# Optimization experiments

Measured on AMD Instinct MI355X. Metric: run time of the kernel, lower is better.

Reference implementation:

```python
import jax, jax.numpy as jnp
import numpy as np

B = 32; SEQ = 900; GRID = 30; PFX = 16; D = 512
H = 8; HD = 64; WS = 3; SS = 1
NW = (GRID // WS) ** 2; N = WS * WS
INTER = 1536  # find_multiple(round(4.0*512*2/3), 256)
EPS = 1e-5
SCALE = HD ** -0.5


def _rel_pos_index():
    coords = np.stack(np.meshgrid(np.arange(WS), np.arange(WS), indexing='ij')).reshape(2, -1)
    rel = (coords[:, :, None] - coords[:, None, :]).transpose(1, 2, 0).copy()
    rel[:, :, 0] += WS - 1
    rel[:, :, 1] += WS - 1
    rel[:, :, 0] *= 2 * WS - 1
    return rel.sum(-1)  # [N, N]


def _attn_mask():
    img = np.zeros((GRID, GRID))
    cnt = 0
    sl = (slice(0, -WS), slice(-WS, -SS), slice(-SS, None))
    for h in sl:
        for w in sl:
            img[h, w] = cnt
            cnt += 1
    mw = img.reshape(GRID // WS, WS, GRID // WS, WS).transpose(0, 2, 1, 3).reshape(-1, N)
    diff = mw[:, None, :] - mw[:, :, None]
    return np.where(diff != 0, -100.0, 0.0).astype(np.float32)  # [nW, N, N]


REL_IDX = _rel_pos_index()
MASK = _attn_mask()


def rms_norm(x):
    xf = x.astype(jnp.float32)
    v = jnp.mean(xf * xf, -1, keepdims=True)
    return (xf * jax.lax.rsqrt(v + EPS)).astype(x.dtype)


def swiglu(x, gu_w, down_w):
    gu = x @ gu_w.T
    gate, up = gu[..., :INTER], gu[..., INTER:]
    return (jax.nn.silu(gate) * up) @ down_w.T


def setup_inputs() -> dict:
    key = jax.random.key(0)
    ks = jax.random.split(key, 8)
    s = 0.02
    return {
        'hidden_states': jax.random.normal(ks[0], (B, PFX + SEQ, D), jnp.float32),
        'qkv_w': jax.random.normal(ks[1], (3 * D, D), jnp.float32) * s,
        'qkv_b': jnp.zeros((3 * D,), jnp.float32),
        'proj_w': jax.random.normal(ks[2], (D, D), jnp.float32) * s,
        'proj_b': jnp.zeros((D,), jnp.float32),
        'rel_bias': jax.random.normal(ks[3], ((2 * WS - 1) ** 2, H), jnp.float32) * s,
        'gu_w': jax.random.normal(ks[4], (2 * INTER, D), jnp.float32) * s,
        'down_w': jax.random.normal(ks[5], (D, INTER), jnp.float32) * s,
        'pgu_w': jax.random.normal(ks[6], (2 * INTER, D), jnp.float32) * s,
        'pdown_w': jax.random.normal(ks[7], (D, INTER), jnp.float32) * s,
    }


def reference(hidden_states, qkv_w, qkv_b, proj_w, proj_b, rel_bias, gu_w, down_w, pgu_w, pdown_w):
    hs = hidden_states
    prefix = hs[:, :PFX]                                     # [B, 16, D]
    grid = hs[:, PFX:] + jnp.mean(prefix, 1, keepdims=True)  # broadcast prefix mean
    x = grid.reshape(B, GRID, GRID, D)
    residual = x
    # cyclic shift
    x = jnp.roll(x, (-SS, -SS), (1, 2))
    # window partition -> [B*nW, N, D]
    xw = x.reshape(B, GRID // WS, WS, GRID // WS, WS, D).transpose(0, 1, 3, 2, 4, 5).reshape(B * NW, N, D)
    qkv = (xw @ qkv_w.T + qkv_b).reshape(B * NW, N, 3, H, HD).transpose(2, 0, 3, 1, 4)
    q, k, v = qkv[0] * SCALE, qkv[1], qkv[2]                 # [B*nW, H, N, HD]
    attn = jnp.einsum('whid,whjd->whij', q, k)
    bias = rel_bias[jnp.asarray(REL_IDX).reshape(-1)].reshape(N, N, H).transpose(2, 0, 1)
    attn = attn + bias[None]
    attn = attn.reshape(B, NW, H, N, N) + jnp.asarray(MASK)[None, :, None]
    attn = jax.nn.softmax(attn.reshape(B * NW, H, N, N), -1)
    out = jnp.einsum('whij,whjd->whid', attn, v).transpose(0, 2, 1, 3).reshape(B * NW, N, D)
    out = out @ proj_w.T + proj_b
    # window reverse + reverse shift
    x = out.reshape(B, GRID // WS, GRID // WS, WS, WS, D).transpose(0, 1, 3, 2, 4, 5).reshape(B, GRID, GRID, D)
    x = jnp.roll(x, (SS, SS), (1, 2))
    x = rms_norm(residual.reshape(B, SEQ, D) + x.reshape(B, SEQ, D))
    prefix = rms_norm(prefix + swiglu(prefix, pgu_w, pdown_w))
    hs = jnp.concatenate([prefix, x], 1)
    return rms_norm(hs + swiglu(hs, gu_w, down_w))
```

## Files before the change

### kernel.cpp

```cpp
#include <hip/hip_runtime.h>
#include <cstdint>
#include <cstddef>

typedef float f32x4 __attribute__((ext_vector_type(4)));
typedef short s16x8 __attribute__((ext_vector_type(8)));
typedef short s16x4 __attribute__((ext_vector_type(4)));

#define DEV static __device__ __forceinline__

DEV float bf2f(short s) {
  union { unsigned u; float f; } c;
  c.u = ((unsigned)(unsigned short)s) << 16;
  return c.f;
}
DEV short f2bf(float f) {
  union { float f; unsigned u; } c;
  c.f = f;
  unsigned r = c.u + 0x7fffu + ((c.u >> 16) & 1u);
  return (short)(r >> 16);
}
DEV float wave_allsum(float v) {
#pragma unroll
  for (int off = 32; off > 0; off >>= 1) v += __shfl_xor(v, off, 64);
  return v;
}
DEV void gload_lds16(const void* g, void* l) {
  __builtin_amdgcn_global_load_lds(
      (const __attribute__((address_space(1))) void*)g,
      (__attribute__((address_space(3))) void*)l, 16, 0, 0);
}
DEV float silu_f(float g) { return g / (1.f + __expf(-g)); }

DEV int xcd_swizzle(int orig, int nwg) {
  int q = nwg >> 3, r = nwg & 7;
  int xcd = orig & 7, pos = orig >> 3;
  return (xcd < r ? xcd * (q + 1) : r * (q + 1) + (xcd - r) * q) + pos;
}

DEV void sync_phase() {
  asm volatile("s_waitcnt vmcnt(0)" ::: "memory");
  __builtin_amdgcn_s_barrier();
  __builtin_amdgcn_sched_barrier(0);
}

enum { EPI_BF16 = 0, EPI_BIAS_BF16 = 1, EPI_SCATTER = 4, EPI_ADDOUT = 5, EPI_GU = 6 };

template <int EPI>
__global__ __launch_bounds__(512, 2) void gemm8(
    const short* __restrict__ A, const short* __restrict__ W,
    const short* __restrict__ Wu, const float* __restrict__ bias,
    void* __restrict__ outp, int M, int N, int K)
{
  __shared__ short lds[65536];
  const int tid = threadIdx.x;
  const int wid = tid >> 6, lane = tid & 63;
  const int wr = wid >> 2, wc = wid & 3;
  const int nwg = gridDim.x * gridDim.y;
  const int orig = blockIdx.y * gridDim.x + blockIdx.x;
  const int wg = xcd_swizzle(orig, nwg);
  const int bx = wg % gridDim.x, by = wg / gridDim.x;
  const int row0 = by * 256;

  f32x4 acc[8][4];
#pragma unroll
  for (int m = 0; m < 8; ++m)
#pragma unroll
    for (int n = 0; n < 4; ++n) acc[m][n] = f32x4{0.f, 0.f, 0.f, 0.f};

  const int srow = tid >> 3;
  const int k8s = (tid & 7) ^ (srow & 7);
  const short* aub[4];
  const short* bub[4];
#pragma unroll
  for (int u = 0; u < 4; ++u)
    aub[u] = A + (size_t)(row0 + u * 64 + srow) * K + k8s * 8;
  if (EPI == EPI_GU) {
    const int colg = bx * 128;
#pragma unroll
    for (int u = 0; u < 2; ++u) {
      bub[u]     = W  + (size_t)(colg + u * 64 + srow) * K + k8s * 8;
      bub[u + 2] = Wu + (size_t)(colg + u * 64 + srow) * K + k8s * 8;
    }
  } else {
    const int c0 = bx * 256;
#pragma unroll
    for (int u = 0; u < 4; ++u)
      bub[u] = W + (size_t)(c0 + u * 64 + srow) * K + k8s * 8;
  }
  const int ldw = wid * 512;

#define SA(d, u, kt) gload_lds16(aub[u] + (kt), &lds[(d)*16384 + (u)*4096 + ldw])
#define SB(d, u, kt) gload_lds16(bub[u] + (kt), &lds[32768 + (d)*16384 + (u)*4096 + ldw])
#define GATE(VN)                                              \
  asm volatile("s_waitcnt vmcnt(" #VN ")" ::: "memory");      \
  __builtin_amdgcn_s_barrier();

  const int kg0 = (lane >> 4) ^ (lane & 7);
  const int kg1 = (4 + (lane >> 4)) ^ (lane & 7);
  const int aoff = (wr * 128 + (lane & 15)) * 64;
  const int boff = 32768 + (wc * 64 + (lane & 15)) * 64;

#define READ_B(d)                                                              \
  _Pragma("unroll") for (int n = 0; n < 4; ++n) {                              \
    bfr[0][n] = *(const s16x8*)&lds[(d)*16384 + boff + n * 1024 + kg0 * 8];    \
    bfr[1][n] = *(const s16x8*)&lds[(d)*16384 + boff + n * 1024 + kg1 * 8];    \
  }
#define DO_PHASE(d, p)                                                         \
  do {                                                                         \
    s16x8 a00 = *(const s16x8*)&lds[(d)*16384 + aoff + (2*(p))*1024 + kg0*8];  \
    s16x8 a01 = *(const s16x8*)&lds[(d)*16384 + aoff + (2*(p))*1024 + kg1*8];  \
    s16x8 a10 = *(const s16x8*)&lds[(d)*16384 + aoff + (2*(p)+1)*1024 + kg0*8];\
    s16x8 a11 = *(const s16x8*)&lds[(d)*16384 + aoff + (2*(p)+1)*1024 + kg1*8];\
    __builtin_amdgcn_s_setprio(1);                                             \
    _Pragma("unroll") for (int n = 0; n < 4; ++n)                              \
      acc[2*(p)][n] = __builtin_amdgcn_mfma_f32_16x16x32_bf16(a00, bfr[0][n], acc[2*(p)][n], 0, 0, 0); \
    _Pragma("unroll") for (int n = 0; n < 4; ++n)                              \
      acc[2*(p)+1][n] = __builtin_amdgcn_mfma_f32_16x16x32_bf16(a10, bfr[0][n], acc[2*(p)+1][n], 0, 0, 0); \
    _Pragma("unroll") for (int n = 0; n < 4; ++n)                              \
      acc[2*(p)][n] = __builtin_amdgcn_mfma_f32_16x16x32_bf16(a01, bfr[1][n], acc[2*(p)][n], 0, 0, 0); \
    _Pragma("unroll") for (int n = 0; n < 4; ++n)                              \
      acc[2*(p)+1][n] = __builtin_amdgcn_mfma_f32_16x16x32_bf16(a11, bfr[1][n], acc[2*(p)+1][n], 0, 0, 0); \
    __builtin_amdgcn_s_setprio(0);                                             \
  } while (0)

  SB(0, 0, 0); SB(0, 1, 0); SB(0, 2, 0); SB(0, 3, 0);
  SA(0, 0, 0); SA(0, 2, 0); SA(0, 1, 0); SA(0, 3, 0);

  const int NT = K >> 6;
  for (int t = 0; t < NT - 1; ++t) {
    const int d = t & 1, d1 = d ^ 1;
    const int kn = (t + 1) * 64;
    s16x8 bfr[2][4];
    SB(d1, 0, kn); SB(d1, 1, kn);
    GATE(4);
    READ_B(d);
    DO_PHASE(d, 0);
    SB(d1, 2, kn); SB(d1, 3, kn);
    DO_PHASE(d, 1);
    SA(d1, 0, kn); SA(d1, 2, kn);
    GATE(6);
    DO_PHASE(d, 2);
    SA(d1, 1, kn); SA(d1, 3, kn);
    DO_PHASE(d, 3);
  }
  {
    const int d = (NT - 1) & 1;
    s16x8 bfr[2][4];
    GATE(2);
    READ_B(d);
    DO_PHASE(d, 0);
    DO_PHASE(d, 1);
    GATE(0);
    DO_PHASE(d, 2);
    DO_PHASE(d, 3);
  }
#undef SA
#undef SB
#undef GATE
#undef READ_B
#undef DO_PHASE

  const int li = lane >> 4, lc = lane & 15;
  if (EPI == EPI_GU) {
    float* fbuf = (float*)lds;
    __syncthreads();
    if (wc >= 2) {
      const int off = (wr * 2 + (wc - 2)) * 8192;
#pragma unroll
      for (int m = 0; m < 8; ++m)
#pragma unroll
        for (int i = 0; i < 4; ++i)
#pragma unroll
          for (int n = 0; n < 4; ++n)
            fbuf[off + (m * 16 + li * 4 + i) * 64 + n * 16 + lc] = acc[m][n][i];
    }
    __syncthreads();
    if (wc < 2) {
      const int off = (wr * 2 + wc) * 8192;
      const int colg = bx * 128;
#pragma unroll
      for (int m = 0; m < 8; ++m) {
#pragma unroll
        for (int i = 0; i < 4; ++i) {
          int gr = row0 + wr * 128 + m * 16 + li * 4 + i;
          if (gr < M) {
#pragma unroll
            for (int n = 0; n < 4; ++n) {
              float u = fbuf[off + (m * 16 + li * 4 + i) * 64 + n * 16 + lc];
              float g = acc[m][n][i];
              ((short*)outp)[(size_t)gr * N + colg + wc * 64 + n * 16 + lc] =
                  f2bf(silu_f(g) * u);
            }
          }
        }
      }
    }
  } else {
    const int c0 = bx * 256;
#pragma unroll
    for (int m = 0; m < 8; ++m) {
#pragma unroll
      for (int i = 0; i < 4; ++i) {
        int gr = row0 + wr * 128 + m * 16 + li * 4 + i;
        if (gr >= M) continue;
        size_t orow;
        if (EPI == EPI_SCATTER) {
          int b = gr / 900, rem = gr % 900;
          int w = rem / 9, n_ = rem % 9;
          int wi = w / 10, wj = w % 10;
          int ii = n_ / 3, jj = n_ % 3;
          int gy = wi * 3 + ii + 1; if (gy >= 30) gy -= 30;
          int gx = wj * 3 + jj + 1; if (gx >= 30) gx -= 30;
          orow = (size_t)b * 900 + gy * 30 + gx;
        } else {
          orow = (size_t)gr;
        }
#pragma unroll
        for (int n = 0; n < 4; ++n) {
          int gc = c0 + wc * 64 + n * 16 + lc;
          float v = acc[m][n][i];
          if (EPI == EPI_BIAS_BF16 || EPI == EPI_SCATTER) v += bias[gc];
          if (EPI == EPI_ADDOUT) {
            float* po = (float*)outp;
            size_t oi = orow * (size_t)N + gc;
            po[oi] = po[oi] + v;
          } else {
            ((short*)outp)[orow * (size_t)N + gc] = f2bf(v);
          }
        }
      }
    }
  }
}

template <int EPI>
__global__ __launch_bounds__(256) void gemm2(
    const short* __restrict__ A, const short* __restrict__ W,
    const short* __restrict__ Wu, const float* __restrict__ bias,
    void* __restrict__ outp, int M, int N, int K)
{
  __shared__ short As0[8192], Bs0[8192];
  __shared__ short As1[8192], Bs1[8192];
  const int tid = threadIdx.x;
  const int wave = tid >> 6, lane = tid & 63;
  const int nwg = gridDim.x * gridDim.y;
  const int orig = blockIdx.y * gridDim.x + blockIdx.x;
  const int wg = xcd_swizzle(orig, nwg);
  const int bx = wg % gridDim.x, by = wg / gridDim.x;
  const int row0 = by * 128;
  const int col0 = (EPI == EPI_GU) ? bx * 64 : bx * 128;
  const int wr = wave >> 1, wc = wave & 1;

  f32x4 acc[4][4];
#pragma unroll
  for (int m = 0; m < 4; ++m)
#pragma unroll
    for (int n = 0; n < 4; ++n) acc[m][n] = f32x4{0.f, 0.f, 0.f, 0.f};

  const short* aptr[4];
  const short* bptr[4];
  int ldst[4];
#pragma unroll
  for (int i = 0; i < 4; ++i) {
    int e = i * 2048 + tid * 8;
    int srow = e >> 6;
    int skg = ((e >> 3) & 7) ^ (srow & 7);
    aptr[i] = A + (size_t)(row0 + srow) * K + skg * 8;
    if (EPI == EPI_GU)
      bptr[i] = (srow < 64 ? W + (size_t)(col0 + srow) * K
                           : Wu + (size_t)(col0 + srow - 64) * K) + skg * 8;
    else
      bptr[i] = W + (size_t)(col0 + srow) * K + skg * 8;
    ldst[i] = i * 2048 + wave * 512;
  }

#define STAGE(AS, BS, KT)                                   \
  do {                                                      \
    _Pragma("unroll") for (int i = 0; i < 4; ++i)           \
        gload_lds16(aptr[i] + (KT), &AS[ldst[i]]);          \
    _Pragma("unroll") for (int i = 0; i < 4; ++i)           \
        gload_lds16(bptr[i] + (KT), &BS[ldst[i]]);          \
  } while (0)

#define COMPUTE(AS, BS)                                                        \
  do {                                                                         \
    _Pragma("unroll") for (int ks = 0; ks < 2; ++ks) {                         \
      s16x8 af[4], bfr[4];                                                     \
      _Pragma("unroll") for (int m = 0; m < 4; ++m) {                          \
        int row = wr * 64 + m * 16 + (lane & 15);                              \
        int kg = (ks * 4 + (lane >> 4)) ^ (row & 7);                           \
        af[m] = *(const s16x8*)&AS[row * 64 + kg * 8];                         \
      }                                                                        \
      _Pragma("unroll") for (int n = 0; n < 4; ++n) {                          \
        int brow = (EPI == EPI_GU)                                             \
                       ? ((n < 2 ? wc * 32 + n * 16                            \
                                 : 64 + wc * 32 + (n - 2) * 16) + (lane & 15)) \
                       : (wc * 64 + n * 16 + (lane & 15));                     \
        int kg = (ks * 4 + (lane >> 4)) ^ (brow & 7);                          \
        bfr[n] = *(const s16x8*)&BS[brow * 64 + kg * 8];                       \
      }                                                                        \
      _Pragma("unroll") for (int m = 0; m < 4; ++m)                            \
          _Pragma("unroll") for (int n = 0; n < 4; ++n)                        \
              acc[m][n] = __builtin_amdgcn_mfma_f32_16x16x32_bf16(             \
                  af[m], bfr[n], acc[m][n], 0, 0, 0);                          \
    }                                                                          \
  } while (0)

  STAGE(As0, Bs0, 0);
  sync_phase();
  for (int kt = 0; kt < K; kt += 128) {
    STAGE(As1, Bs1, kt + 64);
    COMPUTE(As0, Bs0);
    sync_phase();
    if (kt + 128 < K) STAGE(As0, Bs0, kt + 128);
    COMPUTE(As1, Bs1);
    if (kt + 128 < K) sync_phase();
  }
#undef STAGE
#undef COMPUTE

  const int lr = (lane >> 4) * 4, lc = lane & 15;
#pragma unroll
  for (int m = 0; m < 4; ++m) {
#pragma unroll
    for (int i = 0; i < 4; ++i) {
      int gr = row0 + wr * 64 + m * 16 + lr + i;
      if (EPI == EPI_GU) {
#pragma unroll
        for (int n = 0; n < 2; ++n) {
          int gc = col0 + wc * 32 + n * 16 + lc;
          float v = silu_f(acc[m][n][i]) * acc[m][n + 2][i];
          ((short*)outp)[(size_t)gr * N + gc] = f2bf(v);
        }
      } else {
#pragma unroll
        for (int n = 0; n < 4; ++n) {
          int gc = col0 + wc * 64 + n * 16 + lc;
          float v = acc[m][n][i];
          ((short*)outp)[(size_t)gr * N + gc] = f2bf(v);
        }
      }
    }
  }
}

__global__ __launch_bounds__(256) void cvt4_kernel(const float* __restrict__ src,
                                                   short* __restrict__ dst, int n4) {
  int i = blockIdx.x * 256 + threadIdx.x;
  if (i >= n4) return;
  f32x4 v = *(const f32x4*)(src + (size_t)i * 4);
  s16x4 o;
#pragma unroll
  for (int e = 0; e < 4; ++e) o[e] = f2bf(v[e]);
  *(s16x4*)(dst + (size_t)i * 4) = o;
}

__global__ __launch_bounds__(256) void prefix_cvt_kernel(const float* __restrict__ hs,
                                                         short* __restrict__ dst) {
  int i = blockIdx.x * 256 + threadIdx.x;
  if (i >= 512 * 128) return;
  int r = i >> 7, c4 = i & 127;
  int b = r >> 4, t = r & 15;
  f32x4 v = *(const f32x4*)(hs + ((size_t)b * 916 + t) * 512 + c4 * 4);
  s16x4 o;
#pragma unroll
  for (int e = 0; e < 4; ++e) o[e] = f2bf(v[e]);
  *(s16x4*)(dst + (size_t)r * 512 + c4 * 4) = o;
}

__global__ __launch_bounds__(512) void mean_kernel(const float* __restrict__ hs,
                                                   float* __restrict__ m) {
  int b = blockIdx.x, d = threadIdx.x;
  float s = 0.f;
#pragma unroll
  for (int t = 0; t < 16; ++t) s += hs[((size_t)b * 916 + t) * 512 + d];
  m[b * 512 + d] = s * (1.f / 16.f);
}

__global__ __launch_bounds__(256) void prep_kernel(const float* __restrict__ hs,
                                                   const float* __restrict__ m,
                                                   short* __restrict__ gridb,
                                                   short* __restrict__ xw) {
  int idx = blockIdx.x * 256 + threadIdx.x;
  if (idx >= 32 * 900 * 128) return;
  int c4 = idx & 127;
  int row = idx >> 7;
  int b = row / 900, rem = row % 900;
  int gy = rem / 30, gx = rem % 30;
  f32x4 v = *(const f32x4*)(hs + ((size_t)b * 916 + 16 + rem) * 512 + c4 * 4);
  f32x4 mm = *(const f32x4*)(m + b * 512 + c4 * 4);
  v += mm;
  s16x4 o;
#pragma unroll
  for (int e = 0; e < 4; ++e) o[e] = f2bf(v[e]);
  *(s16x4*)(gridb + (size_t)row * 512 + c4 * 4) = o;
  int ry = gy + 29; if (ry >= 30) ry -= 30;
  int rx = gx + 29; if (rx >= 30) rx -= 30;
  int wi = ry / 3, ii = ry % 3, wj = rx / 3, jj = rx % 3;
  size_t xrow = (size_t)((b * 100 + wi * 10 + wj) * 9 + ii * 3 + jj);
  *(s16x4*)(xw + xrow * 512 + c4 * 4) = o;
}

__global__ __launch_bounds__(256) void attn_kernel(const short* __restrict__ qkv,
                                                   const float* __restrict__ rel_bias,
                                                   short* __restrict__ outp) {
  __shared__ short sq[9 * 512];
  __shared__ short sk[9 * 512];
  __shared__ short sv[9 * 512];
  __shared__ float sS[648];
  const int wlin = blockIdx.x;
  const int w = wlin % 100;
  const int wi = w / 10, wj = w % 10;
  const int tid = threadIdx.x;
  const short* base = qkv + (size_t)wlin * 9 * 1536;
  for (int idx = tid; idx < 1728; idx += 256) {
    int n = idx / 192, c8 = idx % 192;
    s16x8 v = *(const s16x8*)(base + (size_t)n * 1536 + c8 * 8);
    int which = c8 >> 6;
    short* dst = (which == 0) ? sq : (which == 1) ? sk : sv;
    *(s16x8*)(dst + n * 512 + (c8 & 63) * 8) = v;
  }
  __syncthreads();
  for (int idx = tid; idx < 648; idx += 256) {
    int h = idx / 81, r = idx % 81, i = r / 9, j = r % 9;
    const short* qp = sq + i * 512 + h * 64;
    const short* kp = sk + j * 512 + h * 64;
    float dot = 0.f;
#pragma unroll
    for (int c = 0; c < 8; ++c) {
      s16x8 qv = *(const s16x8*)(qp + c * 8);
      s16x8 kv = *(const s16x8*)(kp + c * 8);
#pragma unroll
      for (int e = 0; e < 8; ++e) dot += bf2f(qv[e]) * bf2f(kv[e]);
    }
    float s = dot * 0.125f;
    int ia = i / 3, ja = i % 3, ib = j / 3, jb = j % 3;
    s += rel_bias[(5 * (ia - ib + 2) + (ja - jb + 2)) * 8 + h];
    int ra = wi * 3 + ia, ca = wj * 3 + ja, rb = wi * 3 + ib, cb = wj * 3 + jb;
    int rga = (ra < 27) ? 0 : (ra < 29) ? 1 : 2;
    int cga = (ca < 27) ? 0 : (ca < 29) ? 1 : 2;
    int rgb = (rb < 27) ? 0 : (rb < 29) ? 1 : 2;
    int cgb = (cb < 27) ? 0 : (cb < 29) ? 1 : 2;
    if (rga * 3 + cga != rgb * 3 + cgb) s -= 100.f;
    sS[idx] = s;
  }
  __syncthreads();
  if (tid < 72) {
    float* row = sS + tid * 9;
    float mx = row[0];
#pragma unroll
    for (int j = 1; j < 9; ++j) mx = fmaxf(mx, row[j]);
    float e[9], sum = 0.f;
#pragma unroll
    for (int j = 0; j < 9; ++j) { e[j] = __expf(row[j] - mx); sum += e[j]; }
    float inv = 1.f / sum;
#pragma unroll
    for (int j = 0; j < 9; ++j) row[j] = e[j] * inv;
  }
  __syncthreads();
  for (int idx = tid; idx < 576; idx += 256) {
    int h = idx / 72, r = idx % 72, i = r / 8, d8 = r % 8;
    const float* p = sS + (h * 9 + i) * 9;
    float a[8] = {0, 0, 0, 0, 0, 0, 0, 0};
#pragma unroll
    for (int j = 0; j < 9; ++j) {
      float pj = p[j];
      s16x8 vv = *(const s16x8*)(sv + j * 512 + h * 64 + d8 * 8);
#pragma unroll
      for (int e = 0; e < 8; ++e) a[e] += pj * bf2f(vv[e]);
    }
    s16x8 o;
#pragma unroll
    for (int e = 0; e < 8; ++e) o[e] = f2bf(a[e]);
    *(s16x8*)(outp + ((size_t)wlin * 9 + i) * 512 + h * 64 + d8 * 8) = o;
  }
}

__global__ __launch_bounds__(64) void addnorm1_kernel(const short* __restrict__ g,
                                                      const short* __restrict__ p,
                                                      float* __restrict__ out,
                                                      short* __restrict__ hsb) {
  int row = blockIdx.x, lane = threadIdx.x;
  size_t off = (size_t)row * 512 + lane * 8;
  s16x8 a8 = *(const s16x8*)(g + off);
  s16x8 b8 = *(const s16x8*)(p + off);
  float x[8];
  float ss = 0.f;
#pragma unroll
  for (int e = 0; e < 8; ++e) {
    x[e] = bf2f(a8[e]) + bf2f(b8[e]);
    ss += x[e] * x[e];
  }
  ss = wave_allsum(ss);
  float sc = rsqrtf(ss * (1.f / 512.f) + 1e-5f);
  int b_ = row / 900, t = row % 900;
  size_t orow = ((size_t)b_ * 916 + 16 + t) * 512 + lane * 8;
  s16x8 o;
#pragma unroll
  for (int e = 0; e < 8; ++e) {
    x[e] *= sc;
    o[e] = f2bf(x[e]);
  }
  *(f32x4*)(out + orow) = f32x4{x[0], x[1], x[2], x[3]};
  *(f32x4*)(out + orow + 4) = f32x4{x[4], x[5], x[6], x[7]};
  *(s16x8*)(hsb + orow) = o;
}

__global__ __launch_bounds__(64) void prefix_addnorm_kernel(const float* __restrict__ hs,
                                                            const short* __restrict__ pd,
                                                            float* __restrict__ out,
                                                            short* __restrict__ hsb) {
  int r = blockIdx.x, lane = threadIdx.x;
  int b = r >> 4, t = r & 15;
  size_t orow = ((size_t)b * 916 + t) * 512;
  f32x4 x[2];
  float ss = 0.f;
#pragma unroll
  for (int i = 0; i < 2; ++i) {
    f32x4 a = *(const f32x4*)(hs + orow + i * 256 + lane * 4);
    s16x4 d = *(const s16x4*)(pd + (size_t)r * 512 + i * 256 + lane * 4);
#pragma unroll
    for (int e = 0; e < 4; ++e) a[e] += bf2f(d[e]);
    x[i] = a;
    ss += a[0] * a[0] + a[1] * a[1] + a[2] * a[2] + a[3] * a[3];
  }
  ss = wave_allsum(ss);
  float sc = rsqrtf(ss * (1.f / 512.f) + 1e-5f);
#pragma unroll
  for (int i = 0; i < 2; ++i) {
    f32x4 y = x[i] * sc;
    *(f32x4*)(out + orow + i * 256 + lane * 4) = y;
    s16x4 o;
#pragma unroll
    for (int e = 0; e < 4; ++e) o[e] = f2bf(y[e]);
    *(s16x4*)(hsb + orow + i * 256 + lane * 4) = o;
  }
}

__global__ __launch_bounds__(64) void final_addnorm_kernel(float* __restrict__ io) {
  int row = blockIdx.x, lane = threadIdx.x;
  size_t off = (size_t)row * 512;
  f32x4 x[2];
  float ss = 0.f;
#pragma unroll
  for (int i = 0; i < 2; ++i) {
    f32x4 a = *(const f32x4*)(io + off + i * 256 + lane * 4);
    x[i] = a;
    ss += a[0] * a[0] + a[1] * a[1] + a[2] * a[2] + a[3] * a[3];
  }
  ss = wave_allsum(ss);
  float sc = rsqrtf(ss * (1.f / 512.f) + 1e-5f);
#pragma unroll
  for (int i = 0; i < 2; ++i)
    *(f32x4*)(io + off + i * 256 + lane * 4) = x[i] * sc;
}

static constexpr size_t OFF_WQKV   = 0;
static constexpr size_t OFF_WPROJ  = 1572864;
static constexpr size_t OFF_WGU    = 2097152;
static constexpr size_t OFF_WDOWN  = 5242880;
static constexpr size_t OFF_WPGU   = 6815744;
static constexpr size_t OFF_WPDOWN = 9961472;
static constexpr size_t OFF_MEAN   = 11534336;
static constexpr size_t OFF_PREFB  = 11599872;
static constexpr size_t OFF_PINTER = 13697024;
static constexpr size_t OFF_PDOUT  = 15269888;
static constexpr size_t OFF_GRIDB  = 16777216;
static constexpr size_t OFF_XW     = 46268416;
static constexpr size_t OFF_QKV    = 75890688;
static constexpr size_t OFF_ATTNO  = OFF_XW;
static constexpr size_t OFF_PROJS  = OFF_QKV;
static constexpr size_t OFF_INTER  = OFF_GRIDB;
static constexpr size_t OFF_HSB    = 164364288;

extern "C" void kernel_launch(void* const* d_in, const int* in_sizes, int n_in,
                              void* d_out, int out_size, void* d_ws, size_t ws_size,
                              hipStream_t stream) {
  const float* hs      = (const float*)d_in[0];
  const float* qkv_w   = (const float*)d_in[1];
  const float* qkv_b   = (const float*)d_in[2];
  const float* proj_w  = (const float*)d_in[3];
  const float* proj_b  = (const float*)d_in[4];
  const float* rel_b   = (const float*)d_in[5];
  const float* gu_w    = (const float*)d_in[6];
  const float* down_w  = (const float*)d_in[7];
  const float* pgu_w   = (const float*)d_in[8];
  const float* pdown_w = (const float*)d_in[9];

  char* ws = (char*)d_ws;
  short* Wqkv   = (short*)(ws + OFF_WQKV);
  short* Wproj  = (short*)(ws + OFF_WPROJ);
  short* Wgu    = (short*)(ws + OFF_WGU);
  short* Wdown  = (short*)(ws + OFF_WDOWN);
  short* Wpgu   = (short*)(ws + OFF_WPGU);
  short* Wpdown = (short*)(ws + OFF_WPDOWN);
  float* meanb  = (float*)(ws + OFF_MEAN);
  short* prefb  = (short*)(ws + OFF_PREFB);
  short* pinter = (short*)(ws + OFF_PINTER);
  short* pdout  = (short*)(ws + OFF_PDOUT);
  short* gridb  = (short*)(ws + OFF_GRIDB);
  short* xw     = (short*)(ws + OFF_XW);
  short* qkvb   = (short*)(ws + OFF_QKV);
  short* attno  = (short*)(ws + OFF_ATTNO);
  short* projs  = (short*)(ws + OFF_PROJS);
  short* interb = (short*)(ws + OFF_INTER);
  short* hsb    = (short*)(ws + OFF_HSB);
  float* outf   = (float*)d_out;

  cvt4_kernel<<<768, 256, 0, stream>>>(qkv_w, Wqkv, 786432 / 4);
  cvt4_kernel<<<256, 256, 0, stream>>>(proj_w, Wproj, 262144 / 4);
  cvt4_kernel<<<1536, 256, 0, stream>>>(gu_w, Wgu, 1572864 / 4);
  cvt4_kernel<<<768, 256, 0, stream>>>(down_w, Wdown, 786432 / 4);
  cvt4_kernel<<<1536, 256, 0, stream>>>(pgu_w, Wpgu, 1572864 / 4);
  cvt4_kernel<<<768, 256, 0, stream>>>(pdown_w, Wpdown, 786432 / 4);
  prefix_cvt_kernel<<<256, 256, 0, stream>>>(hs, prefb);

  mean_kernel<<<32, 512, 0, stream>>>(hs, meanb);
  prep_kernel<<<14400, 256, 0, stream>>>(hs, meanb, gridb, xw);

  gemm8<EPI_BIAS_BF16><<<dim3(6, 113), 512, 0, stream>>>(
      xw, Wqkv, nullptr, qkv_b, qkvb, 28800, 1536, 512);
  attn_kernel<<<3200, 256, 0, stream>>>(qkvb, rel_b, attno);

  gemm8<EPI_SCATTER><<<dim3(2, 113), 512, 0, stream>>>(
      attno, Wproj, nullptr, proj_b, projs, 28800, 512, 512);
  addnorm1_kernel<<<28800, 64, 0, stream>>>(gridb, projs, outf, hsb);

  gemm2<EPI_GU><<<dim3(24, 4), 256, 0, stream>>>(
      prefb, Wpgu, Wpgu + 1536 * 512, nullptr, pinter, 512, 1536, 512);
  gemm2<EPI_BF16><<<dim3(4, 4), 256, 0, stream>>>(
      pinter, Wpdown, nullptr, nullptr, pdout, 512, 512, 1536);
  prefix_addnorm_kernel<<<512, 64, 0, stream>>>(hs, pdout, outf, hsb);

  gemm8<EPI_GU><<<dim3(12, 115), 512, 0, stream>>>(
      hsb, Wgu, Wgu + 1536 * 512, nullptr, interb, 29312, 1536, 512);
  gemm8<EPI_ADDOUT><<<dim3(2, 115), 512, 0, stream>>>(
      interb, Wdown, nullptr, nullptr, outf, 29312, 512, 1536);
  final_addnorm_kernel<<<29312, 64, 0, stream>>>(outf);

  (void)in_sizes; (void)n_in; (void)out_size; (void)ws_size;
}
```

Baseline: 490.1 us.

## Split gate-up GEMM into dedicated kernel, merge weight casts, drop grid copy

Adds a dedicated gemm8gu kernel. Each wave computes matching gate and up tiles in its own registers and applies SiLU*up directly, so the LDS round-trip and the extra barriers of the old fused epilogue go away. The six weight-conversion launches are merged into one kernel. The separate bf16 grid copy is removed: addnorm1 now reads the residual from the windowed xw buffer through index remapping, and attention output moves to its own buffer. This saves a write pass and some launches, at the cost of more scattered residual reads and a different scheduling balance in the GU kernel.

New measurement: 441.3 us. -10.0%, faster.

```diff
diff --git a/kernel.cpp b/kernel.cpp
--- a/kernel.cpp
+++ b/kernel.cpp
@@ -48,8 +48,8 @@
 template <int EPI>
 __global__ __launch_bounds__(512, 2) void gemm8(
     const short* __restrict__ A, const short* __restrict__ W,
-    const short* __restrict__ Wu, const float* __restrict__ bias,
-    void* __restrict__ outp, int M, int N, int K)
+    const float* __restrict__ bias, void* __restrict__ outp,
+    int M, int N, int K)
 {
   __shared__ short lds[65536];
   const int tid = threadIdx.x;
@@ -60,6 +60,7 @@
   const int wg = xcd_swizzle(orig, nwg);
   const int bx = wg % gridDim.x, by = wg / gridDim.x;
   const int row0 = by * 256;
+  const int c0 = bx * 256;
 
   f32x4 acc[8][4];
 #pragma unroll
@@ -72,20 +73,9 @@
   const short* aub[4];
   const short* bub[4];
 #pragma unroll
-  for (int u = 0; u < 4; ++u)
+  for (int u = 0; u < 4; ++u) {
     aub[u] = A + (size_t)(row0 + u * 64 + srow) * K + k8s * 8;
-  if (EPI == EPI_GU) {
-    const int colg = bx * 128;
-#pragma unroll
-    for (int u = 0; u < 2; ++u) {
-      bub[u]     = W  + (size_t)(colg + u * 64 + srow) * K + k8s * 8;
-      bub[u + 2] = Wu + (size_t)(colg + u * 64 + srow) * K + k8s * 8;
-    }
-  } else {
-    const int c0 = bx * 256;
-#pragma unroll
-    for (int u = 0; u < 4; ++u)
-      bub[u] = W + (size_t)(c0 + u * 64 + srow) * K + k8s * 8;
+    bub[u] = W + (size_t)(c0 + u * 64 + srow) * K + k8s * 8;
   }
   const int ldw = wid * 512;
 
@@ -93,7 +83,8 @@
 #define SB(d, u, kt) gload_lds16(bub[u] + (kt), &lds[32768 + (d)*16384 + (u)*4096 + ldw])
 #define GATE(VN)                                              \
   asm volatile("s_waitcnt vmcnt(" #VN ")" ::: "memory");      \
-  __builtin_amdgcn_s_barrier();
+  __builtin_amdgcn_s_barrier();                               \
+  __builtin_amdgcn_sched_barrier(0);
 
   const int kg0 = (lane >> 4) ^ (lane & 7);
   const int kg1 = (4 + (lane >> 4)) ^ (lane & 7);
@@ -156,78 +147,169 @@
   }
 #undef SA
 #undef SB
-#undef GATE
 #undef READ_B
 #undef DO_PHASE
 
   const int li = lane >> 4, lc = lane & 15;
-  if (EPI == EPI_GU) {
-    float* fbuf = (float*)lds;
-    __syncthreads();
-    if (wc >= 2) {
-      const int off = (wr * 2 + (wc - 2)) * 8192;
-#pragma unroll
-      for (int m = 0; m < 8; ++m)
-#pragma unroll
-        for (int i = 0; i < 4; ++i)
-#pragma unroll
-          for (int n = 0; n < 4; ++n)
-            fbuf[off + (m * 16 + li * 4 + i) * 64 + n * 16 + lc] = acc[m][n][i];
-    }
-    __syncthreads();
-    if (wc < 2) {
-      const int off = (wr * 2 + wc) * 8192;
-      const int colg = bx * 128;
-#pragma unroll
-      for (int m = 0; m < 8; ++m) {
-#pragma unroll
-        for (int i = 0; i < 4; ++i) {
-          int gr = row0 + wr * 128 + m * 16 + li * 4 + i;
-          if (gr < M) {
-#pragma unroll
-            for (int n = 0; n < 4; ++n) {
-              float u = fbuf[off + (m * 16 + li * 4 + i) * 64 + n * 16 + lc];
-              float g = acc[m][n][i];
-              ((short*)outp)[(size_t)gr * N + colg + wc * 64 + n * 16 + lc] =
-                  f2bf(silu_f(g) * u);
-            }
-          }
+#pragma unroll
+  for (int m = 0; m < 8; ++m) {
+#pragma unroll
+    for (int i = 0; i < 4; ++i) {
+      int gr = row0 + wr * 128 + m * 16 + li * 4 + i;
+      if (gr >= M) continue;
+      size_t orow;
+      if (EPI == EPI_SCATTER) {
+        int b = gr / 900, rem = gr % 900;
+        int w = rem / 9, n_ = rem % 9;
+        int wi = w / 10, wj = w % 10;
+        int ii = n_ / 3, jj = n_ % 3;
+        int gy = wi * 3 + ii + 1; if (gy >= 30) gy -= 30;
+        int gx = wj * 3 + jj + 1; if (gx >= 30) gx -= 30;
+        orow = (size_t)b * 900 + gy * 30 + gx;
+      } else {
+        orow = (size_t)gr;
+      }
+#pragma unroll
+      for (int n = 0; n < 4; ++n) {
+        int gc = c0 + wc * 64 + n * 16 + lc;
+        float v = acc[m][n][i];
+        if (EPI == EPI_BIAS_BF16 || EPI == EPI_SCATTER) v += bias[gc];
+        if (EPI == EPI_ADDOUT) {
+          float* po = (float*)outp;
+          size_t oi = orow * (size_t)N + gc;
+          po[oi] = po[oi] + v;
+        } else {
+          ((short*)outp)[orow * (size_t)N + gc] = f2bf(v);
         }
       }
     }
-  } else {
-    const int c0 = bx * 256;
-#pragma unroll
-    for (int m = 0; m < 8; ++m) {
-#pragma unroll
-      for (int i = 0; i < 4; ++i) {
-        int gr = row0 + wr * 128 + m * 16 + li * 4 + i;
-        if (gr >= M) continue;
-        size_t orow;
-        if (EPI == EPI_SCATTER) {
-          int b = gr / 900, rem = gr % 900;
-          int w = rem / 9, n_ = rem % 9;
-          int wi = w / 10, wj = w % 10;
-          int ii = n_ / 3, jj = n_ % 3;
-          int gy = wi * 3 + ii + 1; if (gy >= 30) gy -= 30;
-          int gx = wj * 3 + jj + 1; if (gx >= 30) gx -= 30;
-          orow = (size_t)b * 900 + gy * 30 + gx;
-        } else {
-          orow = (size_t)gr;
-        }
-#pragma unroll
-        for (int n = 0; n < 4; ++n) {
-          int gc = c0 + wc * 64 + n * 16 + lc;
-          float v = acc[m][n][i];
-          if (EPI == EPI_BIAS_BF16 || EPI == EPI_SCATTER) v += bias[gc];
-          if (EPI == EPI_ADDOUT) {
-            float* po = (float*)outp;
-            size_t oi = orow * (size_t)N + gc;
-            po[oi] = po[oi] + v;
-          } else {
-            ((short*)outp)[orow * (size_t)N + gc] = f2bf(v);
-          }
-        }
+  }
+}
+
+__global__ __launch_bounds__(512, 2) void gemm8gu(
+    const short* __restrict__ A, const short* __restrict__ Wg,
+    const short* __restrict__ Wu, short* __restrict__ outp, int M, int K)
+{
+  __shared__ short lds[65536];
+  const int tid = threadIdx.x;
+  const int wid = tid >> 6, lane = tid & 63;
+  const int wr = wid >> 1, wc = wid & 1;
+  const int nwg = gridDim.x * gridDim.y;
+  const int orig = blockIdx.y * gridDim.x + blockIdx.x;
+  const int wg = xcd_swizzle(orig, nwg);
+  const int bx = wg % gridDim.x, by = wg / gridDim.x;
+  const int row0 = by * 256;
+  const int colg = bx * 128;
+
+  f32x4 accg[4][4], accu[4][4];
+#pragma unroll
+  for (int m = 0; m < 4; ++m)
+#pragma unroll
+    for (int n = 0; n < 4; ++n) {
+      accg[m][n] = f32x4{0.f, 0.f, 0.f, 0.f};
+      accu[m][n] = f32x4{0.f, 0.f, 0.f, 0.f};
+    }
+
+  const int srow = tid >> 3;
+  const int k8s = (tid & 7) ^ (srow & 7);
+  const short* aub[4];
+  const short* bub[4];
+#pragma unroll
+  for (int u = 0; u < 4; ++u)
+    aub[u] = A + (size_t)(row0 + u * 64 + srow) * K + k8s * 8;
+#pragma unroll
+  for (int u = 0; u < 2; ++u) {
+    bub[u]     = Wg + (size_t)(colg + u * 64 + srow) * K + k8s * 8;
+    bub[u + 2] = Wu + (size_t)(colg + u * 64 + srow) * K + k8s * 8;
+  }
+  const int ldw = wid * 512;
+
+#define SA(d, u, kt) gload_lds16(aub[u] + (kt), &lds[(d)*16384 + (u)*4096 + ldw])
+#define SB(d, u, kt) gload_lds16(bub[u] + (kt), &lds[32768 + (d)*16384 + (u)*4096 + ldw])
+
+  const int kg0 = (lane >> 4) ^ (lane & 7);
+  const int kg1 = (4 + (lane >> 4)) ^ (lane & 7);
+  const int aoff = (wr * 64 + (lane & 15)) * 64;
+  const int bgoff = 32768 + (wc * 64 + (lane & 15)) * 64;
+  const int buoff = 32768 + (128 + wc * 64 + (lane & 15)) * 64;
+
+#define READ_BF(d, BOFF)                                                       \
+  _Pragma("unroll") for (int n = 0; n < 4; ++n) {                              \
+    bfr[0][n] = *(const s16x8*)&lds[(d)*16384 + (BOFF) + n * 1024 + kg0 * 8];  \
+    bfr[1][n] = *(const s16x8*)&lds[(d)*16384 + (BOFF) + n * 1024 + kg1 * 8];  \
+  }
+#define PHASE2(d, p, ACC)                                                      \
+  do {                                                                         \
+    s16x8 a00 = *(const s16x8*)&lds[(d)*16384 + aoff + (2*(p))*1024 + kg0*8];  \
+    s16x8 a01 = *(const s16x8*)&lds[(d)*16384 + aoff + (2*(p))*1024 + kg1*8];  \
+    s16x8 a10 = *(const s16x8*)&lds[(d)*16384 + aoff + (2*(p)+1)*1024 + kg0*8];\
+    s16x8 a11 = *(const s16x8*)&lds[(d)*16384 + aoff + (2*(p)+1)*1024 + kg1*8];\
+    __builtin_amdgcn_s_setprio(1);                                             \
+    _Pragma("unroll") for (int n = 0; n < 4; ++n)                              \
+      ACC[2*(p)][n] = __builtin_amdgcn_mfma_f32_16x16x32_bf16(a00, bfr[0][n], ACC[2*(p)][n], 0, 0, 0); \
+    _Pragma("unroll") for (int n = 0; n < 4; ++n)                              \
+      ACC[2*(p)+1][n] = __builtin_amdgcn_mfma_f32_16x16x32_bf16(a10, bfr[0][n], ACC[2*(p)+1][n], 0, 0, 0); \
+    _Pragma("unroll") for (int n = 0; n < 4; ++n)                              \
+      ACC[2*(p)][n] = __builtin_amdgcn_mfma_f32_16x16x32_bf16(a01, bfr[1][n], ACC[2*(p)][n], 0, 0, 0); \
+    _Pragma("unroll") for (int n = 0; n < 4; ++n)                              \
+      ACC[2*(p)+1][n] = __builtin_amdgcn_mfma_f32_16x16x32_bf16(a11, bfr[1][n], ACC[2*(p)+1][n], 0, 0, 0); \
+    __builtin_amdgcn_s_setprio(0);                                             \
+  } while (0)
+#define GATE(VN)                                              \
+  asm volatile("s_waitcnt vmcnt(" #VN ")" ::: "memory");      \
+  __builtin_amdgcn_s_barrier();                               \
+  __builtin_amdgcn_sched_barrier(0);
+
+  SA(0, 0, 0); SA(0, 1, 0); SA(0, 2, 0); SA(0, 3, 0);
+  SB(0, 0, 0); SB(0, 1, 0); SB(0, 2, 0); SB(0, 3, 0);
+
+  const int NT = K >> 6;
+  for (int t = 0; t < NT - 1; ++t) {
+    const int d = t & 1, d1 = d ^ 1;
+    const int kn = (t + 1) * 64;
+    s16x8 bfr[2][4];
+    GATE(2);
+    READ_BF(d, bgoff);
+    PHASE2(d, 0, accg);
+    SA(d1, 0, kn); SA(d1, 1, kn);
+    PHASE2(d, 1, accg);
+    SA(d1, 2, kn); SA(d1, 3, kn);
+    GATE(4);
+    READ_BF(d, buoff);
+    PHASE2(d, 0, accu);
+    SB(d1, 0, kn); SB(d1, 1, kn);
+    PHASE2(d, 1, accu);
+    SB(d1, 2, kn); SB(d1, 3, kn);
+  }
+  {
+    const int d = (NT - 1) & 1;
+    s16x8 bfr[2][4];
+    GATE(2);
+    READ_BF(d, bgoff);
+    PHASE2(d, 0, accg);
+    PHASE2(d, 1, accg);
+    GATE(0);
+    READ_BF(d, buoff);
+    PHASE2(d, 0, accu);
+    PHASE2(d, 1, accu);
+  }
+#undef SA
+#undef SB
+#undef READ_BF
+#undef PHASE2
+#undef GATE
+
+  const int li = lane >> 4, lc = lane & 15;
+#pragma unroll
+  for (int m = 0; m < 4; ++m) {
+#pragma unroll
+    for (int i = 0; i < 4; ++i) {
+      int gr = row0 + wr * 64 + m * 16 + li * 4 + i;
+      if (gr >= M) continue;
+#pragma unroll
+      for (int n = 0; n < 4; ++n) {
+        int gc = colg + wc * 64 + n * 16 + lc;
+        outp[(size_t)gr * 1536 + gc] = f2bf(silu_f(accg[m][n][i]) * accu[m][n][i]);
       }
     }
   }
@@ -336,19 +418,33 @@
 #pragma unroll
         for (int n = 0; n < 4; ++n) {
           int gc = col0 + wc * 64 + n * 16 + lc;
-          float v = acc[m][n][i];
-          ((short*)outp)[(size_t)gr * N + gc] = f2bf(v);
+          ((short*)outp)[(size_t)gr * N + gc] = f2bf(acc[m][n][i]);
         }
       }
     }
   }
 }
 
-__global__ __launch_bounds__(256) void cvt4_kernel(const float* __restrict__ src,
-                                                   short* __restrict__ dst, int n4) {
+__global__ __launch_bounds__(256) void cvt_all_kernel(
+    const float* __restrict__ s_qkv, const float* __restrict__ s_proj,
+    const float* __restrict__ s_gu, const float* __restrict__ s_down,
+    const float* __restrict__ s_pgu, const float* __restrict__ s_pdown,
+    short* __restrict__ dst) {
   int i = blockIdx.x * 256 + threadIdx.x;
-  if (i >= n4) return;
-  f32x4 v = *(const f32x4*)(src + (size_t)i * 4);
+  if (i >= 1441792) return;
+  const float* src;
+  int base;
+  if (i < 262144) {
+    if (i < 196608) { src = s_qkv; base = 0; }
+    else            { src = s_proj; base = 196608; }
+  } else if (i < 851968) {
+    if (i < 655360) { src = s_gu; base = 262144; }
+    else            { src = s_down; base = 655360; }
+  } else {
+    if (i < 1245184) { src = s_pgu; base = 851968; }
+    else             { src = s_pdown; base = 1245184; }
+  }
+  f32x4 v = *(const f32x4*)(src + (size_t)(i - base) * 4);
   s16x4 o;
 #pragma unroll
   for (int e = 0; e < 4; ++e) o[e] = f2bf(v[e]);
@@ -379,7 +475,6 @@
 
 __global__ __launch_bounds__(256) void prep_kernel(const float* __restrict__ hs,
                                                    const float* __restrict__ m,
-                                                   short* __restrict__ gridb,
                                                    short* __restrict__ xw) {
   int idx = blockIdx.x * 256 + threadIdx.x;
   if (idx >= 32 * 900 * 128) return;
@@ -390,14 +485,13 @@
   f32x4 v = *(const f32x4*)(hs + ((size_t)b * 916 + 16 + rem) * 512 + c4 * 4);
   f32x4 mm = *(const f32x4*)(m + b * 512 + c4 * 4);
   v += mm;
-  s16x4 o;
-#pragma unroll
-  for (int e = 0; e < 4; ++e) o[e] = f2bf(v[e]);
-  *(s16x4*)(gridb + (size_t)row * 512 + c4 * 4) = o;
   int ry = gy + 29; if (ry >= 30) ry -= 30;
   int rx = gx + 29; if (rx >= 30) rx -= 30;
   int wi = ry / 3, ii = ry % 3, wj = rx / 3, jj = rx % 3;
   size_t xrow = (size_t)((b * 100 + wi * 10 + wj) * 9 + ii * 3 + jj);
+  s16x4 o;
+#pragma unroll
+  for (int e = 0; e < 4; ++e) o[e] = f2bf(v[e]);
   *(s16x4*)(xw + xrow * 512 + c4 * 4) = o;
 }
 
@@ -476,14 +570,18 @@
   }
 }
 
-__global__ __launch_bounds__(64) void addnorm1_kernel(const short* __restrict__ g,
+__global__ __launch_bounds__(64) void addnorm1_kernel(const short* __restrict__ xw,
                                                       const short* __restrict__ p,
                                                       float* __restrict__ out,
                                                       short* __restrict__ hsb) {
   int row = blockIdx.x, lane = threadIdx.x;
-  size_t off = (size_t)row * 512 + lane * 8;
-  s16x8 a8 = *(const s16x8*)(g + off);
-  s16x8 b8 = *(const s16x8*)(p + off);
+  int b_ = row / 900, rem = row % 900;
+  int gy = rem / 30, gx = rem % 30;
+  int ry = gy + 29; if (ry >= 30) ry -= 30;
+  int rx = gx + 29; if (rx >= 30) rx -= 30;
+  size_t xrow = (size_t)((b_ * 100 + (ry / 3) * 10 + rx / 3) * 9 + (ry % 3) * 3 + rx % 3);
+  s16x8 a8 = *(const s16x8*)(xw + xrow * 512 + lane * 8);
+  s16x8 b8 = *(const s16x8*)(p + (size_t)row * 512 + lane * 8);
   float x[8];
   float ss = 0.f;
 #pragma unroll
@@ -493,8 +591,7 @@
   }
   ss = wave_allsum(ss);
   float sc = rsqrtf(ss * (1.f / 512.f) + 1e-5f);
-  int b_ = row / 900, t = row % 900;
-  size_t orow = ((size_t)b_ * 916 + 16 + t) * 512 + lane * 8;
+  size_t orow = ((size_t)b_ * 916 + 16 + rem) * 512 + lane * 8;
   s16x8 o;
 #pragma unroll
   for (int e = 0; e < 8; ++e) {
@@ -565,12 +662,11 @@
 static constexpr size_t OFF_PREFB  = 11599872;
 static constexpr size_t OFF_PINTER = 13697024;
 static constexpr size_t OFF_PDOUT  = 15269888;
-static constexpr size_t OFF_GRIDB  = 16777216;
-static constexpr size_t OFF_XW     = 46268416;
-static constexpr size_t OFF_QKV    = 75890688;
-static constexpr size_t OFF_ATTNO  = OFF_XW;
+static constexpr size_t OFF_XW     = 16777216;
+static constexpr size_t OFF_QKV    = 46399488;
+static constexpr size_t OFF_ATTNO  = 134873088;
 static constexpr size_t OFF_PROJS  = OFF_QKV;
-static constexpr size_t OFF_INTER  = OFF_GRIDB;
+static constexpr size_t OFF_INTER  = OFF_XW;
 static constexpr size_t OFF_HSB    = 164364288;
 
 extern "C" void kernel_launch(void* const* d_in, const int* in_sizes, int n_in,
@@ -598,7 +694,6 @@
   short* prefb  = (short*)(ws + OFF_PREFB);
   short* pinter = (short*)(ws + OFF_PINTER);
   short* pdout  = (short*)(ws + OFF_PDOUT);
-  short* gridb  = (short*)(ws + OFF_GRIDB);
   short* xw     = (short*)(ws + OFF_XW);
   short* qkvb   = (short*)(ws + OFF_QKV);
   short* attno  = (short*)(ws + OFF_ATTNO);
@@ -607,24 +702,20 @@
   short* hsb    = (short*)(ws + OFF_HSB);
   float* outf   = (float*)d_out;
 
-  cvt4_kernel<<<768, 256, 0, stream>>>(qkv_w, Wqkv, 786432 / 4);
-  cvt4_kernel<<<256, 256, 0, stream>>>(proj_w, Wproj, 262144 / 4);
-  cvt4_kernel<<<1536, 256, 0, stream>>>(gu_w, Wgu, 1572864 / 4);
-  cvt4_kernel<<<768, 256, 0, stream>>>(down_w, Wdown, 786432 / 4);
-  cvt4_kernel<<<1536, 256, 0, stream>>>(pgu_w, Wpgu, 1572864 / 4);
-  cvt4_kernel<<<768, 256, 0, stream>>>(pdown_w, Wpdown, 786432 / 4);
+  cvt_all_kernel<<<5632, 256, 0, stream>>>(qkv_w, proj_w, gu_w, down_w,
+                                           pgu_w, pdown_w, (short*)ws);
   prefix_cvt_kernel<<<256, 256, 0, stream>>>(hs, prefb);
 
   mean_kernel<<<32, 512, 0, stream>>>(hs, meanb);
-  prep_kernel<<<14400, 256, 0, stream>>>(hs, meanb, gridb, xw);
+  prep_kernel<<<14400, 256, 0, stream>>>(hs, meanb, xw);
 
   gemm8<EPI_BIAS_BF16><<<dim3(6, 113), 512, 0, stream>>>(
-      xw, Wqkv, nullptr, qkv_b, qkvb, 28800, 1536, 512);
+      xw, Wqkv, qkv_b, qkvb, 28800, 1536, 512);
   attn_kernel<<<3200, 256, 0, stream>>>(qkvb, rel_b, attno);
 
   gemm8<EPI_SCATTER><<<dim3(2, 113), 512, 0, stream>>>(
-      attno, Wproj, nullptr, proj_b, projs, 28800, 512, 512);
-  addnorm1_kernel<<<28800, 64, 0, stream>>>(gridb, projs, outf, hsb);
+      attno, Wproj, proj_b, projs, 28800, 512, 512);
+  addnorm1_kernel<<<28800, 64, 0, stream>>>(xw, projs, outf, hsb);
 
   gemm2<EPI_GU><<<dim3(24, 4), 256, 0, stream>>>(
       prefb, Wpgu, Wpgu + 1536 * 512, nullptr, pinter, 512, 1536, 512);
@@ -632,10 +723,10 @@
       pinter, Wpdown, nullptr, nullptr, pdout, 512, 512, 1536);
   prefix_addnorm_kernel<<<512, 64, 0, stream>>>(hs, pdout, outf, hsb);
 
-  gemm8<EPI_GU><<<dim3(12, 115), 512, 0, stream>>>(
-      hsb, Wgu, Wgu + 1536 * 512, nullptr, interb, 29312, 1536, 512);
+  gemm8gu<<<dim3(12, 115), 512, 0, stream>>>(
+      hsb, Wgu, Wgu + 1536 * 512, interb, 29312, 512);
   gemm8<EPI_ADDOUT><<<dim3(2, 115), 512, 0, stream>>>(
-      interb, Wdown, nullptr, nullptr, outf, 29312, 512, 1536);
+      interb, Wdown, nullptr, outf, 29312, 512, 1536);
   final_addnorm_kernel<<<29312, 64, 0, stream>>>(outf);
 
   (void)in_sizes; (void)n_in; (void)out_size; (void)ws_size;
```
